# Performance work log

Hardware: AMD Instinct MI355X
Metric: run time of the kernel (lower is better)

## Reference

```python
import jax, jax.numpy as jnp
import numpy as np

LOG2 = 0.6931471805599453

def logcosh(x):
    # numerically stable log(cosh(x)) = |x| + log1p(exp(-2|x|)) - log(2)
    ax = jnp.abs(x)
    return ax + jnp.log1p(jnp.exp(-2.0 * ax)) - LOG2

def setup_inputs() -> dict:
    key = jax.random.key(0)
    k1, k2, k3 = jax.random.split(key, 3)
    B, N, G, F = 16384, 1024, 256, 16  # batch, n_sites, n_symm, alpha_symm
    # each row of perms is a valid permutation of [0, N)
    perms = jax.vmap(lambda k: jax.random.permutation(k, N))(jax.random.split(k1, G)).astype(jnp.int32)
    x = jax.random.normal(k2, (B, N), dtype=jnp.float32)
    W = jax.random.normal(k3, (N, F), dtype=jnp.float32) * 0.1  # kernel_init = normal(0.1)
    b = jnp.zeros((F,), dtype=jnp.float32)
    v_bias = jnp.zeros((1,), dtype=jnp.float32)
    return {"x": x, "W": W, "b": b, "v_bias": v_bias, "perms": perms}

def reference(x, W, b, v_bias, perms):
    # scan over group permutations: gather x by perm, matmul, bias, logcosh, sum
    def f(carry, perm):
        y = x[..., perm] @ W + b          # [B, F]
        return carry + jnp.sum(logcosh(y), axis=-1), None
    y0 = jnp.zeros(x.shape[:-1], dtype=x.dtype)
    y_out, _ = jax.lax.scan(f, y0, perms)
    y_out = y_out + v_bias[0] * jnp.sum(x, axis=-1)
    return y_out
```

## Files before the change

### kernel.cpp

```cpp
#include <hip/hip_runtime.h>
#include <math.h>

typedef __bf16 bf16x8 __attribute__((ext_vector_type(8)));
typedef float f32x4 __attribute__((ext_vector_type(4)));


__device__ __forceinline__ unsigned short f2bf(float f) {
    unsigned int u = __float_as_uint(f);
    u += 0x7FFFu + ((u >> 16) & 1u);
    return (unsigned short)(u >> 16);
}

__device__ __forceinline__ float logcosh_fast(float v) {
    float a = fabsf(v);
    float t = __expf(-2.0f * a);
    return a + (__logf(1.0f + t) - 0.6931471805599453f);
}

template <int CTRL>
__device__ __forceinline__ float dppadd(float x) {
    int y = __builtin_amdgcn_update_dpp(0, __float_as_int(x), CTRL, 0xf, 0xf, true);
    return x + __int_as_float(y);
}

__device__ __forceinline__ void gload_lds16(const void* g, void* l) {
    __builtin_amdgcn_global_load_lds(
        (__attribute__((address_space(1))) void*)(void*)g,
        (__attribute__((address_space(3))) void*)l, 16, 0, 0);
}

#define SBAR()  __builtin_amdgcn_s_barrier()
#define SCHED() __builtin_amdgcn_sched_barrier(0)

__global__ __launch_bounds__(256) void k_invert(const int* __restrict__ perms,
                                                int* __restrict__ inv) {
    int t = blockIdx.x * 256 + threadIdx.x;
    int g = t >> 10, n = t & 1023;
    inv[(g << 10) + perms[t]] = n;
}

__global__ __launch_bounds__(256) void k_build_bt(const float* __restrict__ W,
                                                  const int* __restrict__ inv,
                                                  unsigned short* __restrict__ bT) {
    int j = blockIdx.x;
    int g = j >> 4, f = j & 15;
    const int* invg = inv + (g << 10);
    size_t rowbase = (size_t)j << 10;
#pragma unroll
    for (int i = 0; i < 4; ++i) {
        int k = (i << 8) + threadIdx.x;
        int n = invg[k];
        bT[rowbase + k] = f2bf(W[(n << 4) + f]);
    }
}

__global__ __launch_bounds__(256) void k_convert(const float* __restrict__ x,
                                                 const float* __restrict__ vb,
                                                 unsigned short* __restrict__ xb,
                                                 float* __restrict__ out) {
    int row = blockIdx.x, tid = threadIdx.x;
    size_t base = ((size_t)row << 10) + (tid << 2);
    float4 v = *reinterpret_cast<const float4*>(x + base);
    ushort4 h;
    h.x = f2bf(v.x); h.y = f2bf(v.y); h.z = f2bf(v.z); h.w = f2bf(v.w);
    *reinterpret_cast<ushort4*>(xb + base) = h;
    float s = v.x + v.y + v.z + v.w;
#pragma unroll
    for (int off = 32; off > 0; off >>= 1) s += __shfl_down(s, off);
    __shared__ float ls[4];
    if ((tid & 63) == 0) ls[tid >> 6] = s;
    __syncthreads();
    if (tid == 0) out[row] = vb[0] * (ls[0] + ls[1] + ls[2] + ls[3]);
}


#define MFMA_M(MM)                                                               \
    _Pragma("unroll") for (int k_ = 0; k_ < 2; ++k_)                             \
    _Pragma("unroll") for (int n_ = 0; n_ < 4; ++n_)                             \
        acc[MM][n_] = __builtin_amdgcn_mfma_f32_16x16x32_bf16(                   \
            aF[MM][k_], bF[n_][k_], acc[MM][n_], 0, 0, 0);

__device__ __forceinline__ void stage_half(unsigned short* dst,
                                           const unsigned short* src, int h,
                                           int tid, int wv) {
#pragma unroll
    for (int j = 0; j < 2; ++j) {
        int c0 = (h * 128 + j * 64) * 8;
        int cc = c0 + tid;
        int r = cc >> 3;
        int cs = (cc & 7) ^ (r & 7);
        gload_lds16(src + (((size_t)r) << 10) + (cs << 3),
                    dst + ((c0 + wv * 64) << 3));
    }
}

template <bool STAGE, int VM>
__device__ __forceinline__ void tile_iter(
    const unsigned short* Ap, const unsigned short* Bp,
    unsigned short* AsD, unsigned short* BsD,
    const unsigned short* xsrc, const unsigned short* bsrc,
    f32x4 (&acc)[8][4], int aRow, int bRow, int po0, int po1, int tid, int wv) {
    bf16x8 aF[8][2], bF[4][2];

#pragma unroll
    for (int n = 0; n < 4; ++n) {
        bF[n][0] = *reinterpret_cast<const bf16x8*>(Bp + bRow + po0 + n * 1024);
        bF[n][1] = *reinterpret_cast<const bf16x8*>(Bp + bRow + po1 + n * 1024);
    }
#pragma unroll
    for (int m = 0; m < 2; ++m) {
        aF[m][0] = *reinterpret_cast<const bf16x8*>(Ap + aRow + po0 + m * 1024);
        aF[m][1] = *reinterpret_cast<const bf16x8*>(Ap + aRow + po1 + m * 1024);
    }
    SCHED();

#pragma unroll
    for (int m = 0; m < 6; ++m) {
        aF[m + 2][0] = *reinterpret_cast<const bf16x8*>(Ap + aRow + po0 + (m + 2) * 1024);
        aF[m + 2][1] = *reinterpret_cast<const bf16x8*>(Ap + aRow + po1 + (m + 2) * 1024);
        SCHED();
        asm volatile("s_waitcnt lgkmcnt(4)" ::: "memory");
        SCHED();
        __builtin_amdgcn_s_setprio(1);
        MFMA_M(m)
        __builtin_amdgcn_s_setprio(0);
        SCHED();
    }

    asm volatile("s_waitcnt lgkmcnt(0)" ::: "memory");
    SCHED();
    SBAR();

    if (STAGE) { stage_half(AsD, xsrc, 0, tid, wv); stage_half(AsD, xsrc, 1, tid, wv); }
    SCHED();
    __builtin_amdgcn_s_setprio(1);
    MFMA_M(6)
    __builtin_amdgcn_s_setprio(0);
    SCHED();

    if (STAGE) { stage_half(BsD, bsrc, 0, tid, wv); stage_half(BsD, bsrc, 1, tid, wv); }
    SCHED();
    __builtin_amdgcn_s_setprio(1);
    MFMA_M(7)
    __builtin_amdgcn_s_setprio(0);
    SCHED();
    if (VM == 8)      { asm volatile("s_waitcnt vmcnt(8)" ::: "memory"); }
    else if (VM == 0) { asm volatile("s_waitcnt vmcnt(0)" ::: "memory"); }
    SCHED();
    SBAR();
}

__global__ __launch_bounds__(512, 2) void k_gemm(const unsigned short* __restrict__ xb,
                                                 const unsigned short* __restrict__ bT,
                                                 const float* __restrict__ bias,
                                                 float* __restrict__ partial, int B) {
    __shared__ unsigned short As[2][256 * 64];
    __shared__ unsigned short Bs[2][256 * 64];

    const int tid = threadIdx.x;
    const int lane = tid & 63;
    const int wv = tid >> 6;
    const int wm = wv >> 2;
    const int wn = wv & 3;
    const int lr = lane & 15;
    const int lk = lane >> 4;

    const int fid = blockIdx.y * gridDim.x + blockIdx.x;
    const int cpx = (gridDim.x * gridDim.y) >> 3;
    const int swz = (fid & 7) * cpx + (fid >> 3);
    const int cbx = swz & 15;
    const int row0 = (swz >> 4) << 8;
    const int j0 = cbx << 8;

    const unsigned short* xbase = xb + ((size_t)row0 << 10);
    const unsigned short* bbase = bT + ((size_t)j0 << 10);

    const int aRow = (wm * 128 + lr) * 64;
    const int bRow = (wn * 64 + lr) * 64;
    const int po0 = (lk ^ (lr & 7)) * 8;
    const int po1 = ((4 + lk) ^ (lr & 7)) * 8;

    f32x4 acc[8][4];
#pragma unroll
    for (int m = 0; m < 8; ++m)
#pragma unroll
        for (int n = 0; n < 4; ++n)
            acc[m][n] = {0.f, 0.f, 0.f, 0.f};

    stage_half(&As[0][0], xbase, 0, tid, wv);
    stage_half(&As[0][0], xbase, 1, tid, wv);
    stage_half(&Bs[0][0], bbase, 0, tid, wv);
    stage_half(&Bs[0][0], bbase, 1, tid, wv);
    stage_half(&As[1][0], xbase + 64, 0, tid, wv);
    stage_half(&As[1][0], xbase + 64, 1, tid, wv);
    stage_half(&Bs[1][0], bbase + 64, 0, tid, wv);
    stage_half(&Bs[1][0], bbase + 64, 1, tid, wv);
    asm volatile("s_waitcnt vmcnt(8)" ::: "memory");
    SCHED();
    SBAR();

    for (int tt = 0; tt < 7; ++tt) {
        const int t0 = tt * 2;
        tile_iter<true, 8>(&As[0][0], &Bs[0][0], &As[0][0], &Bs[0][0],
                           xbase + ((t0 + 2) << 6), bbase + ((t0 + 2) << 6),
                           acc, aRow, bRow, po0, po1, tid, wv);
        tile_iter<true, 8>(&As[1][0], &Bs[1][0], &As[1][0], &Bs[1][0],
                           xbase + ((t0 + 3) << 6), bbase + ((t0 + 3) << 6),
                           acc, aRow, bRow, po0, po1, tid, wv);
    }
    tile_iter<false, 0>(&As[0][0], &Bs[0][0], &As[0][0], &Bs[0][0],
                        xbase, bbase, acc, aRow, bRow, po0, po1, tid, wv);
    tile_iter<false, -1>(&As[1][0], &Bs[1][0], &As[1][0], &Bs[1][0],
                         xbase, bbase, acc, aRow, bRow, po0, po1, tid, wv);

    float* rowsum = (float*)&As[0][0];
    const float bv = bias[lr];
#pragma unroll
    for (int m = 0; m < 8; ++m) {
#pragma unroll
        for (int r = 0; r < 4; ++r) {
            float s = 0.f;
#pragma unroll
            for (int n = 0; n < 4; ++n) s += logcosh_fast(acc[m][n][r] + bv);
            s = dppadd<0x111>(s);
            s = dppadd<0x112>(s);
            s = dppadd<0x114>(s);
            s = dppadd<0x118>(s);
            if (lr == 15)
                rowsum[wn * 256 + wm * 128 + m * 16 + lk * 4 + r] = s;
        }
    }
    __syncthreads();
    if (tid < 256) {
        float s = rowsum[tid] + rowsum[256 + tid] + rowsum[512 + tid] + rowsum[768 + tid];
        partial[(size_t)cbx * B + row0 + tid] = s;
    }
}

__global__ __launch_bounds__(256) void k_final(const float* __restrict__ partial,
                                               float* __restrict__ out, int ncb, int B) {
    int b = blockIdx.x * 256 + threadIdx.x;
    float s = out[b];
    for (int c = 0; c < ncb; ++c) s += partial[(size_t)c * B + b];
    out[b] = s;
}

extern "C" void kernel_launch(void* const* d_in, const int* in_sizes, int n_in,
                              void* d_out, int out_size, void* d_ws, size_t ws_size,
                              hipStream_t stream) {
    const float* x      = (const float*)d_in[0];
    const float* W      = (const float*)d_in[1];
    const float* bias   = (const float*)d_in[2];
    const float* v_bias = (const float*)d_in[3];
    const int*   perms  = (const int*)d_in[4];
    float* out = (float*)d_out;

    const int N  = 1024;
    const int B  = in_sizes[0] / N;
    const int G  = in_sizes[4] / N;
    const int GF = G * 16;
    const int NCB = GF / 256;

    char* w = (char*)d_ws;
    unsigned short* xb = (unsigned short*)w;
    unsigned short* bT = (unsigned short*)(w + (size_t)B * N * 2);
    int* inv = (int*)(w + (size_t)B * N * 2 + (size_t)GF * N * 2);
    float* partial = (float*)(w + (size_t)B * N * 2 + (size_t)GF * N * 2
                              + (size_t)G * N * 4);

    k_invert<<<G * N / 256, 256, 0, stream>>>(perms, inv);
    k_build_bt<<<GF, 256, 0, stream>>>(W, inv, bT);
    k_convert<<<B, 256, 0, stream>>>(x, v_bias, xb, out);
    k_gemm<<<dim3(NCB, B / 256), 512, 0, stream>>>(xb, bT, bias, partial, B);
    k_final<<<B / 256, 256, 0, stream>>>(partial, out, NCB, B);
}
```

Baseline: 188.4 us.

## Switch GEMM core from 16x16x32 to 32x32x16 bf16 MFMA tiles

Replaces the 16x16x32 MFMA tiling with 32x32x16 MFMA instructions, so each wave now holds 4x2 accumulator blocks of 16 floats. Fragment loads, LDS swizzle offsets, staging address precomputation and the epilogue row-sum reduction (an extra DPP row-broadcast step) are rewritten to match the 32-lane layout. The larger MFMA shape cuts the number of LDS fragment reads and MFMA issues per tile, at the cost of a different register pressure profile and a more intricate epilogue index mapping.

```diff
diff --git a/kernel.cpp b/kernel.cpp
--- a/kernel.cpp
+++ b/kernel.cpp
@@ -2,7 +2,7 @@
 #include <math.h>
 
 typedef __bf16 bf16x8 __attribute__((ext_vector_type(8)));
-typedef float f32x4 __attribute__((ext_vector_type(4)));
+typedef float f32x16 __attribute__((ext_vector_type(16)));
 
 
 __device__ __forceinline__ unsigned short f2bf(float f) {
@@ -74,74 +74,76 @@
 }
 
 
-#define MFMA_M(MM)                                                               \
-    _Pragma("unroll") for (int k_ = 0; k_ < 2; ++k_)                             \
-    _Pragma("unroll") for (int n_ = 0; n_ < 4; ++n_)                             \
-        acc[MM][n_] = __builtin_amdgcn_mfma_f32_16x16x32_bf16(                   \
-            aF[MM][k_], bF[n_][k_], acc[MM][n_], 0, 0, 0);
-
-__device__ __forceinline__ void stage_half(unsigned short* dst,
-                                           const unsigned short* src, int h,
-                                           int tid, int wv) {
-#pragma unroll
-    for (int j = 0; j < 2; ++j) {
-        int c0 = (h * 128 + j * 64) * 8;
-        int cc = c0 + tid;
-        int r = cc >> 3;
-        int cs = (cc & 7) ^ (r & 7);
-        gload_lds16(src + (((size_t)r) << 10) + (cs << 3),
-                    dst + ((c0 + wv * 64) << 3));
-    }
+__device__ __forceinline__ void stage_i(unsigned short* dst, const unsigned short* src,
+                                        int voff, int i, int wv) {
+    gload_lds16(src + voff, dst + (((i << 9) + (wv << 6)) << 3));
 }
 
 template <bool STAGE, int VM>
-__device__ __forceinline__ void tile_iter(
+__device__ __forceinline__ void tile32(
     const unsigned short* Ap, const unsigned short* Bp,
     unsigned short* AsD, unsigned short* BsD,
     const unsigned short* xsrc, const unsigned short* bsrc,
-    f32x4 (&acc)[8][4], int aRow, int bRow, int po0, int po1, int tid, int wv) {
-    bf16x8 aF[8][2], bF[4][2];
-
-#pragma unroll
-    for (int n = 0; n < 4; ++n) {
-        bF[n][0] = *reinterpret_cast<const bf16x8*>(Bp + bRow + po0 + n * 1024);
-        bF[n][1] = *reinterpret_cast<const bf16x8*>(Bp + bRow + po1 + n * 1024);
-    }
-#pragma unroll
-    for (int m = 0; m < 2; ++m) {
-        aF[m][0] = *reinterpret_cast<const bf16x8*>(Ap + aRow + po0 + m * 1024);
-        aF[m][1] = *reinterpret_cast<const bf16x8*>(Ap + aRow + po1 + m * 1024);
-    }
-    SCHED();
-
-#pragma unroll
-    for (int m = 0; m < 6; ++m) {
-        aF[m + 2][0] = *reinterpret_cast<const bf16x8*>(Ap + aRow + po0 + (m + 2) * 1024);
-        aF[m + 2][1] = *reinterpret_cast<const bf16x8*>(Ap + aRow + po1 + (m + 2) * 1024);
+    f32x16 (&acc)[4][2], const int (&vs)[4],
+    int aBase, int bBase, const int (&po)[4], int wv) {
+    bf16x8 aF[2][4], bF[2][4];
+
+#pragma unroll
+    for (int nb = 0; nb < 2; ++nb)
+#pragma unroll
+        for (int s = 0; s < 4; ++s)
+            bF[nb][s] = *reinterpret_cast<const bf16x8*>(Bp + bBase + nb * 2048 + po[s]);
+#pragma unroll
+    for (int s = 0; s < 4; ++s)
+        aF[0][s] = *reinterpret_cast<const bf16x8*>(Ap + aBase + po[s]);
+    SCHED();
+
+#pragma unroll
+    for (int mb = 0; mb < 3; ++mb) {
+#pragma unroll
+        for (int s = 0; s < 4; ++s)
+            aF[(mb + 1) & 1][s] = *reinterpret_cast<const bf16x8*>(
+                Ap + aBase + (mb + 1) * 2048 + po[s]);
         SCHED();
         asm volatile("s_waitcnt lgkmcnt(4)" ::: "memory");
         SCHED();
         __builtin_amdgcn_s_setprio(1);
-        MFMA_M(m)
+#pragma unroll
+        for (int s = 0; s < 4; ++s)
+#pragma unroll
+            for (int nb = 0; nb < 2; ++nb)
+                acc[mb][nb] = __builtin_amdgcn_mfma_f32_32x32x16_bf16(
+                    aF[mb & 1][s], bF[nb][s], acc[mb][nb], 0, 0, 0);
         __builtin_amdgcn_s_setprio(0);
         SCHED();
     }
-
     asm volatile("s_waitcnt lgkmcnt(0)" ::: "memory");
     SCHED();
     SBAR();
 
-    if (STAGE) { stage_half(AsD, xsrc, 0, tid, wv); stage_half(AsD, xsrc, 1, tid, wv); }
+    if (STAGE) {
+#pragma unroll
+        for (int i = 0; i < 4; ++i) stage_i(AsD, xsrc, vs[i], i, wv);
+    }
     SCHED();
     __builtin_amdgcn_s_setprio(1);
-    MFMA_M(6)
+#pragma unroll
+    for (int s = 0; s < 4; ++s)
+        acc[3][0] = __builtin_amdgcn_mfma_f32_32x32x16_bf16(
+            aF[1][s], bF[0][s], acc[3][0], 0, 0, 0);
     __builtin_amdgcn_s_setprio(0);
     SCHED();
 
-    if (STAGE) { stage_half(BsD, bsrc, 0, tid, wv); stage_half(BsD, bsrc, 1, tid, wv); }
+    if (STAGE) {
+#pragma unroll
+        for (int i = 0; i < 4; ++i) stage_i(BsD, bsrc, vs[i], i, wv);
+    }
     SCHED();
     __builtin_amdgcn_s_setprio(1);
-    MFMA_M(7)
+#pragma unroll
+    for (int s = 0; s < 4; ++s)
+        acc[3][1] = __builtin_amdgcn_mfma_f32_32x32x16_bf16(
+            aF[1][s], bF[1][s], acc[3][1], 0, 0, 0);
     __builtin_amdgcn_s_setprio(0);
     SCHED();
     if (VM == 8)      { asm volatile("s_waitcnt vmcnt(8)" ::: "memory"); }
@@ -162,8 +164,8 @@
     const int wv = tid >> 6;
     const int wm = wv >> 2;
     const int wn = wv & 3;
-    const int lr = lane & 15;
-    const int lk = lane >> 4;
+    const int la31 = lane & 31;
+    const int hi = lane >> 5;
 
     const int fid = blockIdx.y * gridDim.x + blockIdx.x;
     const int cpx = (gridDim.x * gridDim.y) >> 3;
@@ -175,59 +177,69 @@
     const unsigned short* xbase = xb + ((size_t)row0 << 10);
     const unsigned short* bbase = bT + ((size_t)j0 << 10);
 
-    const int aRow = (wm * 128 + lr) * 64;
-    const int bRow = (wn * 64 + lr) * 64;
-    const int po0 = (lk ^ (lr & 7)) * 8;
-    const int po1 = ((4 + lk) ^ (lr & 7)) * 8;
-
-    f32x4 acc[8][4];
-#pragma unroll
-    for (int m = 0; m < 8; ++m)
-#pragma unroll
-        for (int n = 0; n < 4; ++n)
-            acc[m][n] = {0.f, 0.f, 0.f, 0.f};
-
-    stage_half(&As[0][0], xbase, 0, tid, wv);
-    stage_half(&As[0][0], xbase, 1, tid, wv);
-    stage_half(&Bs[0][0], bbase, 0, tid, wv);
-    stage_half(&Bs[0][0], bbase, 1, tid, wv);
-    stage_half(&As[1][0], xbase + 64, 0, tid, wv);
-    stage_half(&As[1][0], xbase + 64, 1, tid, wv);
-    stage_half(&Bs[1][0], bbase + 64, 0, tid, wv);
-    stage_half(&Bs[1][0], bbase + 64, 1, tid, wv);
+    const int aBase = (wm * 128 + la31) * 64;
+    const int bBase = (wn * 64 + la31) * 64;
+    int po[4];
+#pragma unroll
+    for (int s = 0; s < 4; ++s) po[s] = ((2 * s + hi) ^ (la31 & 7)) * 8;
+
+    int vs[4];
+#pragma unroll
+    for (int i = 0; i < 4; ++i) {
+        int cc = (i << 9) + tid;
+        int r = cc >> 3;
+        int cs = (cc & 7) ^ (r & 7);
+        vs[i] = (r << 10) + (cs << 3);
+    }
+
+    f32x16 acc[4][2];
+#pragma unroll
+    for (int mb = 0; mb < 4; ++mb)
+#pragma unroll
+        for (int nb = 0; nb < 2; ++nb)
+#pragma unroll
+            for (int i = 0; i < 16; ++i) acc[mb][nb][i] = 0.f;
+
+#pragma unroll
+    for (int i = 0; i < 4; ++i) stage_i(&As[0][0], xbase, vs[i], i, wv);
+#pragma unroll
+    for (int i = 0; i < 4; ++i) stage_i(&Bs[0][0], bbase, vs[i], i, wv);
+#pragma unroll
+    for (int i = 0; i < 4; ++i) stage_i(&As[1][0], xbase + 64, vs[i], i, wv);
+#pragma unroll
+    for (int i = 0; i < 4; ++i) stage_i(&Bs[1][0], bbase + 64, vs[i], i, wv);
     asm volatile("s_waitcnt vmcnt(8)" ::: "memory");
     SCHED();
     SBAR();
 
     for (int tt = 0; tt < 7; ++tt) {
         const int t0 = tt * 2;
-        tile_iter<true, 8>(&As[0][0], &Bs[0][0], &As[0][0], &Bs[0][0],
-                           xbase + ((t0 + 2) << 6), bbase + ((t0 + 2) << 6),
-                           acc, aRow, bRow, po0, po1, tid, wv);
-        tile_iter<true, 8>(&As[1][0], &Bs[1][0], &As[1][0], &Bs[1][0],
-                           xbase + ((t0 + 3) << 6), bbase + ((t0 + 3) << 6),
-                           acc, aRow, bRow, po0, po1, tid, wv);
-    }
-    tile_iter<false, 0>(&As[0][0], &Bs[0][0], &As[0][0], &Bs[0][0],
-                        xbase, bbase, acc, aRow, bRow, po0, po1, tid, wv);
-    tile_iter<false, -1>(&As[1][0], &Bs[1][0], &As[1][0], &Bs[1][0],
-                         xbase, bbase, acc, aRow, bRow, po0, po1, tid, wv);
+        tile32<true, 8>(&As[0][0], &Bs[0][0], &As[0][0], &Bs[0][0],
+                        xbase + ((t0 + 2) << 6), bbase + ((t0 + 2) << 6),
+                        acc, vs, aBase, bBase, po, wv);
+        tile32<true, 8>(&As[1][0], &Bs[1][0], &As[1][0], &Bs[1][0],
+                        xbase + ((t0 + 3) << 6), bbase + ((t0 + 3) << 6),
+                        acc, vs, aBase, bBase, po, wv);
+    }
+    tile32<false, 0>(&As[0][0], &Bs[0][0], &As[0][0], &Bs[0][0],
+                     xbase, bbase, acc, vs, aBase, bBase, po, wv);
+    tile32<false, -1>(&As[1][0], &Bs[1][0], &As[1][0], &Bs[1][0],
+                      xbase, bbase, acc, vs, aBase, bBase, po, wv);
 
     float* rowsum = (float*)&As[0][0];
-    const float bv = bias[lr];
-#pragma unroll
-    for (int m = 0; m < 8; ++m) {
-#pragma unroll
-        for (int r = 0; r < 4; ++r) {
-            float s = 0.f;
-#pragma unroll
-            for (int n = 0; n < 4; ++n) s += logcosh_fast(acc[m][n][r] + bv);
+    const float bv = bias[lane & 15];
+#pragma unroll
+    for (int mb = 0; mb < 4; ++mb) {
+#pragma unroll
+        for (int i = 0; i < 16; ++i) {
+            float s = logcosh_fast(acc[mb][0][i] + bv) + logcosh_fast(acc[mb][1][i] + bv);
             s = dppadd<0x111>(s);
             s = dppadd<0x112>(s);
             s = dppadd<0x114>(s);
             s = dppadd<0x118>(s);
-            if (lr == 15)
-                rowsum[wn * 256 + wm * 128 + m * 16 + lk * 4 + r] = s;
+            s = dppadd<0x142>(s);
+            if (la31 == 31)
+                rowsum[wn * 256 + wm * 128 + mb * 32 + (i & 3) + 8 * (i >> 2) + 4 * hi] = s;
         }
     }
     __syncthreads();
```

Measured after the change: 205.7 us. 9.2% more time.

## Restructure GEMM double-buffer pipeline to issue next-tile loads at iteration start

Applied to the files above, without the earlier changes.

Changes the LDS double-buffering so each iteration issues the global-to-LDS copies for the next tile into the other buffer at the start, instead of waiting for all LDS reads and a barrier mid-iteration before staging into the buffer just consumed. This removes one barrier per iteration and gives the async loads the whole iteration to land. The per-thread source offsets are precomputed once into registers. In exchange it waits vmcnt(0) at each iteration end, so load latency is only hidden inside one tile's compute, and it holds four extra offset registers.

```diff
diff --git a/kernel.cpp b/kernel.cpp
--- a/kernel.cpp
+++ b/kernel.cpp
@@ -80,28 +80,27 @@
         acc[MM][n_] = __builtin_amdgcn_mfma_f32_16x16x32_bf16(                   \
             aF[MM][k_], bF[n_][k_], acc[MM][n_], 0, 0, 0);
 
-__device__ __forceinline__ void stage_half(unsigned short* dst,
-                                           const unsigned short* src, int h,
-                                           int tid, int wv) {
-#pragma unroll
-    for (int j = 0; j < 2; ++j) {
-        int c0 = (h * 128 + j * 64) * 8;
-        int cc = c0 + tid;
-        int r = cc >> 3;
-        int cs = (cc & 7) ^ (r & 7);
-        gload_lds16(src + (((size_t)r) << 10) + (cs << 3),
-                    dst + ((c0 + wv * 64) << 3));
-    }
-}
-
-template <bool STAGE, int VM>
-__device__ __forceinline__ void tile_iter(
+__device__ __forceinline__ void stage_i(unsigned short* dst, const unsigned short* src,
+                                        int voff, int i, int wv) {
+    gload_lds16(src + voff, dst + (((i << 9) + (wv << 6)) << 3));
+}
+
+template <bool ST, int VM>
+__device__ __forceinline__ void tile_fs(
     const unsigned short* Ap, const unsigned short* Bp,
     unsigned short* AsD, unsigned short* BsD,
     const unsigned short* xsrc, const unsigned short* bsrc,
-    f32x4 (&acc)[8][4], int aRow, int bRow, int po0, int po1, int tid, int wv) {
+    f32x4 (&acc)[8][4], const int (&vs)[4],
+    int aRow, int bRow, int po0, int po1, int wv) {
     bf16x8 aF[8][2], bF[4][2];
 
+    if (ST) {
+#pragma unroll
+        for (int i = 0; i < 4; ++i) stage_i(AsD, xsrc, vs[i], i, wv);
+#pragma unroll
+        for (int i = 0; i < 4; ++i) stage_i(BsD, bsrc, vs[i], i, wv);
+    }
+    SCHED();
 #pragma unroll
     for (int n = 0; n < 4; ++n) {
         bF[n][0] = *reinterpret_cast<const bf16x8*>(Bp + bRow + po0 + n * 1024);
@@ -126,26 +125,19 @@
         __builtin_amdgcn_s_setprio(0);
         SCHED();
     }
-
-    asm volatile("s_waitcnt lgkmcnt(0)" ::: "memory");
-    SCHED();
-    SBAR();
-
-    if (STAGE) { stage_half(AsD, xsrc, 0, tid, wv); stage_half(AsD, xsrc, 1, tid, wv); }
+    asm volatile("s_waitcnt lgkmcnt(2)" ::: "memory");
     SCHED();
     __builtin_amdgcn_s_setprio(1);
     MFMA_M(6)
     __builtin_amdgcn_s_setprio(0);
     SCHED();
-
-    if (STAGE) { stage_half(BsD, bsrc, 0, tid, wv); stage_half(BsD, bsrc, 1, tid, wv); }
+    asm volatile("s_waitcnt lgkmcnt(0)" ::: "memory");
     SCHED();
     __builtin_amdgcn_s_setprio(1);
     MFMA_M(7)
     __builtin_amdgcn_s_setprio(0);
     SCHED();
-    if (VM == 8)      { asm volatile("s_waitcnt vmcnt(8)" ::: "memory"); }
-    else if (VM == 0) { asm volatile("s_waitcnt vmcnt(0)" ::: "memory"); }
+    if (VM == 0) { asm volatile("s_waitcnt vmcnt(0)" ::: "memory"); }
     SCHED();
     SBAR();
 }
@@ -180,6 +172,15 @@
     const int po0 = (lk ^ (lr & 7)) * 8;
     const int po1 = ((4 + lk) ^ (lr & 7)) * 8;
 
+    int vs[4];
+#pragma unroll
+    for (int i = 0; i < 4; ++i) {
+        int cc = (i << 9) + tid;
+        int r = cc >> 3;
+        int cs = (cc & 7) ^ (r & 7);
+        vs[i] = (r << 10) + (cs << 3);
+    }
+
     f32x4 acc[8][4];
 #pragma unroll
     for (int m = 0; m < 8; ++m)
@@ -187,31 +188,31 @@
         for (int n = 0; n < 4; ++n)
             acc[m][n] = {0.f, 0.f, 0.f, 0.f};
 
-    stage_half(&As[0][0], xbase, 0, tid, wv);
-    stage_half(&As[0][0], xbase, 1, tid, wv);
-    stage_half(&Bs[0][0], bbase, 0, tid, wv);
-    stage_half(&Bs[0][0], bbase, 1, tid, wv);
-    stage_half(&As[1][0], xbase + 64, 0, tid, wv);
-    stage_half(&As[1][0], xbase + 64, 1, tid, wv);
-    stage_half(&Bs[1][0], bbase + 64, 0, tid, wv);
-    stage_half(&Bs[1][0], bbase + 64, 1, tid, wv);
+#pragma unroll
+    for (int i = 0; i < 4; ++i) stage_i(&As[0][0], xbase, vs[i], i, wv);
+#pragma unroll
+    for (int i = 0; i < 4; ++i) stage_i(&Bs[0][0], bbase, vs[i], i, wv);
+#pragma unroll
+    for (int i = 0; i < 4; ++i) stage_i(&As[1][0], xbase + 64, vs[i], i, wv);
+#pragma unroll
+    for (int i = 0; i < 4; ++i) stage_i(&Bs[1][0], bbase + 64, vs[i], i, wv);
     asm volatile("s_waitcnt vmcnt(8)" ::: "memory");
     SCHED();
     SBAR();
 
+    tile_fs<false, 0>(&As[0][0], &Bs[0][0], &As[1][0], &Bs[1][0],
+                      xbase, bbase, acc, vs, aRow, bRow, po0, po1, wv);
     for (int tt = 0; tt < 7; ++tt) {
-        const int t0 = tt * 2;
-        tile_iter<true, 8>(&As[0][0], &Bs[0][0], &As[0][0], &Bs[0][0],
-                           xbase + ((t0 + 2) << 6), bbase + ((t0 + 2) << 6),
-                           acc, aRow, bRow, po0, po1, tid, wv);
-        tile_iter<true, 8>(&As[1][0], &Bs[1][0], &As[1][0], &Bs[1][0],
-                           xbase + ((t0 + 3) << 6), bbase + ((t0 + 3) << 6),
-                           acc, aRow, bRow, po0, po1, tid, wv);
-    }
-    tile_iter<false, 0>(&As[0][0], &Bs[0][0], &As[0][0], &Bs[0][0],
-                        xbase, bbase, acc, aRow, bRow, po0, po1, tid, wv);
-    tile_iter<false, -1>(&As[1][0], &Bs[1][0], &As[1][0], &Bs[1][0],
-                         xbase, bbase, acc, aRow, bRow, po0, po1, tid, wv);
+        const int t = 2 * tt + 1;
+        tile_fs<true, 0>(&As[1][0], &Bs[1][0], &As[0][0], &Bs[0][0],
+                         xbase + ((t + 1) << 6), bbase + ((t + 1) << 6),
+                         acc, vs, aRow, bRow, po0, po1, wv);
+        tile_fs<true, 0>(&As[0][0], &Bs[0][0], &As[1][0], &Bs[1][0],
+                         xbase + ((t + 2) << 6), bbase + ((t + 2) << 6),
+                         acc, vs, aRow, bRow, po0, po1, wv);
+    }
+    tile_fs<false, -1>(&As[1][0], &Bs[1][0], &As[0][0], &Bs[0][0],
+                       xbase, bbase, acc, vs, aRow, bRow, po0, po1, wv);
 
     float* rowsum = (float*)&As[0][0];
     const float bv = bias[lr];
```

Result: no change. 190.1 us (+0.9%).
